# Performance work log

Hardware: AMD Instinct MI355X
Metric: run time of the kernel (lower is better)

## Reference

```python
import jax, jax.numpy as jnp
import numpy as np
from jax import lax

DIM = 128
HEADS = 8
HEAD_DIM = DIM // HEADS
SR = 2
B, H, W = 2, 80, 80
SCALE = HEAD_DIM ** (-0.5)
BN_EPS = 1e-5


def _conv1x1(x, w, b):
    # x: (B,C,H,W), w: (O,C), b: (O,)
    return jnp.einsum('bchw,oc->bohw', x, w) + b[None, :, None, None]


def setup_inputs() -> dict:
    key = jax.random.key(0)
    ks = jax.random.split(key, 12)
    s = DIM ** -0.5
    x = jax.random.normal(ks[0], (B, DIM, H, W), dtype=jnp.float32)
    q_w = jax.random.normal(ks[1], (DIM, DIM), dtype=jnp.float32) * s
    q_b = jnp.zeros((DIM,), jnp.float32)
    k_w = jax.random.normal(ks[2], (DIM, DIM), dtype=jnp.float32) * s
    k_b = jnp.zeros((DIM,), jnp.float32)
    v_w = jax.random.normal(ks[3], (DIM, DIM), dtype=jnp.float32) * s
    v_b = jnp.zeros((DIM,), jnp.float32)
    sr_w = jax.random.normal(ks[4], (DIM, DIM, SR, SR), dtype=jnp.float32) * (s / SR)
    sr_b = jnp.zeros((DIM,), jnp.float32)
    bn_gamma = jnp.ones((DIM,), jnp.float32)
    bn_beta = jnp.zeros((DIM,), jnp.float32)
    bn_mean = jnp.zeros((DIM,), jnp.float32)
    bn_var = jnp.ones((DIM,), jnp.float32)
    proj_w = jax.random.normal(ks[5], (DIM, DIM), dtype=jnp.float32) * s
    proj_b = jnp.zeros((DIM,), jnp.float32)
    return dict(x=x, q_w=q_w, q_b=q_b, k_w=k_w, k_b=k_b, v_w=v_w, v_b=v_b,
                sr_w=sr_w, sr_b=sr_b, bn_gamma=bn_gamma, bn_beta=bn_beta,
                bn_mean=bn_mean, bn_var=bn_var, proj_w=proj_w, proj_b=proj_b)


def reference(x, q_w, q_b, k_w, k_b, v_w, v_b, sr_w, sr_b,
              bn_gamma, bn_beta, bn_mean, bn_var, proj_w, proj_b):
    b, c, h, w = x.shape
    n = h * w
    # q: (B,h,N,d)
    q = _conv1x1(x, q_w, q_b).reshape(b, HEADS, HEAD_DIM, n).transpose(0, 1, 3, 2)
    # spatial reduction: Conv2d(k=SR, s=SR) + BN(eval) + ReLU
    x_kv = lax.conv_general_dilated(x, sr_w, window_strides=(SR, SR),
                                    padding='VALID',
                                    dimension_numbers=('NCHW', 'OIHW', 'NCHW'))
    x_kv = x_kv + sr_b[None, :, None, None]
    inv = bn_gamma / jnp.sqrt(bn_var + BN_EPS)
    x_kv = x_kv * inv[None, :, None, None] + (bn_beta - bn_mean * inv)[None, :, None, None]
    x_kv = jax.nn.relu(x_kv)
    n_kv = x_kv.shape[2] * x_kv.shape[3]
    k = _conv1x1(x_kv, k_w, k_b).reshape(b, HEADS, HEAD_DIM, n_kv).transpose(0, 1, 3, 2)
    v = _conv1x1(x_kv, v_w, v_b).reshape(b, HEADS, HEAD_DIM, n_kv).transpose(0, 1, 3, 2)
    # explicit attention: (B,h,N,N_kv)
    attn = jnp.einsum('bhnd,bhmd->bhnm', q, k) * SCALE
    attn = jax.nn.softmax(attn, axis=-1)
    out = jnp.einsum('bhnm,bhmd->bhnd', attn, v)  # (B,h,N,d)
    # faithful to source layout: transpose(1,2) then reshape to (B,C,H,W)
    out = out.transpose(0, 2, 1, 3).reshape(b, c, h, w)
    out = _conv1x1(out, proj_w, proj_b)
    return out
```

## Files before the change

### kernel.cpp

```cpp
#include <hip/hip_runtime.h>
#include <hip/hip_bf16.h>
#include <cmath>

#define DIM 128
#define HEADS 8
#define NBATCH 2
#define NQ 6400
#define NKV 1600
#define NC 50
#define BN_EPS 1e-5f
#define LOG2E 1.4426950408889634f

typedef __bf16 bf16_t;
typedef __attribute__((ext_vector_type(8))) __bf16 bf16x8;
typedef __attribute__((ext_vector_type(16))) float f32x16;

union BF8U { bf16x8 v; unsigned u[4]; };

__device__ inline unsigned packbf2(float a, float b) {
  union { __hip_bfloat162 v; unsigned u; } r;
  r.v = __float22bfloat162_rn(make_float2(a, b));
  return r.u;
}

__device__ inline unsigned short f2bf(float v) {
  unsigned u = __float_as_uint(v);
  return (unsigned short)((u + 0x7FFFu + ((u >> 16) & 1u)) >> 16);
}

__global__ __launch_bounds__(256) void mgemm_qsrkv(
    const float* __restrict__ x,
    const float* __restrict__ qw, const float* __restrict__ kw,
    const float* __restrict__ vw, const float* __restrict__ srw,
    const float* __restrict__ q_b, const float* __restrict__ sr_b,
    const float* __restrict__ k_b, const float* __restrict__ v_b,
    const float* __restrict__ bng, const float* __restrict__ bnb,
    const float* __restrict__ bnm, const float* __restrict__ bnv,
    unsigned short* __restrict__ Qb,
    unsigned short* __restrict__ Kp, unsigned short* __restrict__ Vp,
    float sl)
{
  __shared__ __align__(16) unsigned short xs4[32][520];
  __shared__ __align__(16) unsigned short xs[32][136];
  int t = threadIdx.x;
  int ln = t & 31, hf = (t >> 5) & 1, wid = t >> 6;
  int b = blockIdx.y;
  int o = wid * 32 + ln;

  if (blockIdx.x < 50) {
    int cid = blockIdx.x;
    int s0 = cid * 32;

    {
      int tx = t & 31, g = t >> 5;
      int s = s0 + tx;
      int i = s / 40, j = s % 40;
      const float* xb = x + (size_t)b * DIM * NQ;
#pragma unroll
      for (int u = 0; u < 32; ++u) {
        int idx2 = g * 32 + u;
        int c = idx2 >> 1, ky = idx2 & 1;
        const float* src = xb + (size_t)c * NQ + (2 * i + ky) * 80 + 2 * j;
        float2 vv = *(const float2*)src;
        *(unsigned*)&xs4[tx][c * 4 + ky * 2] = packbf2(vv.x, vv.y);
      }
    }
    __syncthreads();

    const unsigned short* arow = &xs4[ln][hf * 8];
    const float* wrow = srw + (size_t)o * 512;
    f32x16 acc = {};
#pragma unroll 8
    for (int c0 = 0; c0 < 512; c0 += 16) {
      int cb = c0 + hf * 8;
      bf16x8 af = *(const bf16x8*)&arow[c0];
      BF8U bf;
      float4 w0 = *(const float4*)(wrow + cb);
      float4 w1 = *(const float4*)(wrow + cb + 4);
      bf.u[0] = packbf2(w0.x, w0.y); bf.u[1] = packbf2(w0.z, w0.w);
      bf.u[2] = packbf2(w1.x, w1.y); bf.u[3] = packbf2(w1.z, w1.w);
      acc = __builtin_amdgcn_mfma_f32_32x32x16_bf16(af, bf.v, acc, 0, 0, 0);
    }
    float bv = sr_b[o];
    float inv = bng[o] / sqrtf(bnv[o] + BN_EPS);
    float b2 = bnb[o] - bnm[o] * inv;
#pragma unroll
    for (int g = 0; g < 4; ++g)
#pragma unroll
      for (int jj = 0; jj < 4; ++jj) {
        int sr = 8 * g + 4 * hf + jj;
        xs[sr][o] = f2bf(fmaxf((acc[4 * g + jj] + bv) * inv + b2, 0.f));
      }
    __syncthreads();

    const unsigned short* ar2 = &xs[ln][hf * 8];
    const float* kwrow = kw + (size_t)o * DIM;
    const float* vwrow = vw + (size_t)o * DIM;
    f32x16 ka = {}, va = {};
#pragma unroll
    for (int c0 = 0; c0 < 128; c0 += 16) {
      int cb = c0 + hf * 8;
      bf16x8 af = *(const bf16x8*)&ar2[c0];
      BF8U kb, vb;
      float4 k0 = *(const float4*)(kwrow + cb);
      float4 k1 = *(const float4*)(kwrow + cb + 4);
      float4 v0 = *(const float4*)(vwrow + cb);
      float4 v1 = *(const float4*)(vwrow + cb + 4);
      kb.u[0] = packbf2(k0.x, k0.y); kb.u[1] = packbf2(k0.z, k0.w);
      kb.u[2] = packbf2(k1.x, k1.y); kb.u[3] = packbf2(k1.z, k1.w);
      vb.u[0] = packbf2(v0.x, v0.y); vb.u[1] = packbf2(v0.z, v0.w);
      vb.u[2] = packbf2(v1.x, v1.y); vb.u[3] = packbf2(v1.z, v1.w);
      ka = __builtin_amdgcn_mfma_f32_32x32x16_bf16(af, kb.v, ka, 0, 0, 0);
      va = __builtin_amdgcn_mfma_f32_32x32x16_bf16(af, vb.v, va, 0, 0, 0);
    }
    int hloc = o >> 4, d = o & 15;
    {
      float kb2 = k_b[o];
      size_t CB = (((size_t)b * HEADS + hloc) * NC + cid) * 512;
#pragma unroll
      for (int g = 0; g < 4; ++g)
#pragma unroll
        for (int jj = 0; jj < 4; ++jj) {
          int sl2 = 8 * g + 4 * hf + jj;
          Kp[CB + sl2 * 16 + d] = f2bf(ka[4 * g + jj] + kb2);
        }
    }
    {
      float vb2 = v_b[o];
      size_t CB = (((size_t)b * HEADS + hloc) * NC + cid) * 1024;
      uint4 w0, w1;
      w0.x = packbf2(va[0] + vb2, va[1] + vb2);
      w0.y = packbf2(va[2] + vb2, va[3] + vb2);
      w0.z = packbf2(va[4] + vb2, va[5] + vb2);
      w0.w = packbf2(va[6] + vb2, va[7] + vb2);
      w1.x = packbf2(va[8] + vb2, va[9] + vb2);
      w1.y = packbf2(va[10] + vb2, va[11] + vb2);
      w1.z = packbf2(va[12] + vb2, va[13] + vb2);
      w1.w = packbf2(va[14] + vb2, va[15] + vb2);
      *(uint4*)&Vp[CB + d * 16 + hf * 8] = w0;
      *(uint4*)&Vp[CB + 512 + d * 16 + hf * 8] = w1;
    }
    {
      int hh = t >> 5, pos = t & 31;
      size_t addr = (((size_t)b * HEADS + hh) * NC + cid) * 1024 + 256 +
                    ((pos & 16) ? 512 : 0) + (pos & 15);
      Vp[addr] = 0x3F80;
    }
  } else {
    int s0 = (blockIdx.x - 50) * 32;

    {
      int tx = t & 31, cg = t >> 5;
      const float* xb = x + (size_t)b * DIM * NQ + s0 + tx;
#pragma unroll
      for (int it = 0; it < 8; ++it) {
        int c = 2 * cg + 16 * it;
        float a0 = xb[(size_t)c * NQ];
        float a1 = xb[(size_t)(c + 1) * NQ];
        *(unsigned*)&xs[tx][c] = packbf2(a0, a1);
      }
    }
    __syncthreads();

    const unsigned short* arow = &xs[ln][hf * 8];
    const float* qwrow = qw + (size_t)o * DIM;
    f32x16 acc = {};
#pragma unroll
    for (int c0 = 0; c0 < 128; c0 += 16) {
      int cb = c0 + hf * 8;
      bf16x8 af = *(const bf16x8*)&arow[c0];
      BF8U bf;
      float4 b0 = *(const float4*)(qwrow + cb);
      float4 b1 = *(const float4*)(qwrow + cb + 4);
      bf.u[0] = packbf2(b0.x, b0.y); bf.u[1] = packbf2(b0.z, b0.w);
      bf.u[2] = packbf2(b1.x, b1.y); bf.u[3] = packbf2(b1.z, b1.w);
      acc = __builtin_amdgcn_mfma_f32_32x32x16_bf16(af, bf.v, acc, 0, 0, 0);
    }
    float bv = q_b[o];
#pragma unroll
    for (int g = 0; g < 4; ++g)
#pragma unroll
      for (int jj = 0; jj < 4; ++jj) {
        int sq = s0 + 8 * g + 4 * hf + jj;
        Qb[((size_t)b * NQ + sq) * DIM + o] = f2bf((acc[4 * g + jj] + bv) * sl);
      }
  }
}

__global__ __launch_bounds__(256) void attn_split(
    const bf16_t* __restrict__ Qb, const bf16_t* __restrict__ Kp,
    const bf16_t* __restrict__ Vp, unsigned short* __restrict__ Pb,
    float* __restrict__ Lsum)
{
  const int t = threadIdx.x;
  const int ln = t & 31, hf = (t >> 5) & 1, wid = t >> 6;
  const int h = blockIdx.y;
  const int b = blockIdx.z & 1, half = blockIdx.z >> 1;
  const int q0 = blockIdx.x * 128 + wid * 32;

  bf16x8 qf = *(const bf16x8*)&Qb[((size_t)b * NQ + q0 + ln) * DIM + h * 16 + hf * 8];
  const int bh = b * HEADS + h;
  const bf16_t* kc = &Kp[((size_t)bh * NC + half * 25) * 512 + ln * 16 + hf * 8];
  const bf16_t* vc = &Vp[((size_t)bh * NC + half * 25) * 1024 + ln * 16 + hf * 8];

  f32x16 acc0 = {}, acc1 = {};
  const f32x16 zero = {};

  bf16x8 kf0 = *(const bf16x8*)kc;
  bf16x8 va0 = *(const bf16x8*)vc;
  bf16x8 vb0 = *(const bf16x8*)(vc + 512);
  bf16x8 kf1 = *(const bf16x8*)(kc + 512);
  bf16x8 va1 = *(const bf16x8*)(vc + 1024);
  bf16x8 vb1 = *(const bf16x8*)(vc + 1536);

  f32x16 S0 = __builtin_amdgcn_mfma_f32_32x32x16_bf16(kf0, qf, zero, 0, 0, 0);

  for (int c = 0; c < 25; ++c) {
    int cn = (c + 2 < 25) ? c + 2 : 24;
    bf16x8 kf2 = *(const bf16x8*)(kc + (size_t)cn * 512);
    bf16x8 va2 = *(const bf16x8*)(vc + (size_t)cn * 1024);
    bf16x8 vb2 = *(const bf16x8*)(vc + (size_t)cn * 1024 + 512);

    f32x16 S1 = __builtin_amdgcn_mfma_f32_32x32x16_bf16(kf1, qf, zero, 0, 0, 0);

    BF8U f0, f1;
#pragma unroll
    for (int i = 0; i < 4; ++i) {
      f0.u[i] = packbf2(__builtin_amdgcn_exp2f(S0[2 * i]),
                        __builtin_amdgcn_exp2f(S0[2 * i + 1]));
      f1.u[i] = packbf2(__builtin_amdgcn_exp2f(S0[8 + 2 * i]),
                        __builtin_amdgcn_exp2f(S0[9 + 2 * i]));
    }

    acc0 = __builtin_amdgcn_mfma_f32_32x32x16_bf16(va0, f0.v, acc0, 0, 0, 0);
    acc1 = __builtin_amdgcn_mfma_f32_32x32x16_bf16(vb0, f1.v, acc1, 0, 0, 0);

    S0 = S1;
    kf0 = kf1; va0 = va1; vb0 = vb1;
    kf1 = kf2; va1 = va2; vb1 = vb2;
  }

  f32x16 acc;
#pragma unroll
  for (int i = 0; i < 16; ++i) acc[i] = acc0[i] + acc1[i];

  unsigned short* prow =
      &Pb[(size_t)(half * 2 + b) * (NQ * DIM) + (size_t)(q0 + ln) * DIM + h * 16 + 4 * hf];
  uint2 w0, w1;
  w0.x = packbf2(acc[0], acc[1]); w0.y = packbf2(acc[2], acc[3]);
  w1.x = packbf2(acc[4], acc[5]); w1.y = packbf2(acc[6], acc[7]);
  *(uint2*)&prow[0] = w0;
  *(uint2*)&prow[8] = w1;
  if (!hf)
    Lsum[(size_t)(half * 2 + b) * (HEADS * NQ) + (size_t)h * NQ + q0 + ln] = acc[8];
}

__global__ __launch_bounds__(256) void proj_comb(
    const unsigned short* __restrict__ Pb, const float* __restrict__ Lsum,
    const float* __restrict__ pw, const float* __restrict__ p_b,
    float* __restrict__ Out)
{
  __shared__ __align__(16) unsigned short As[32][136];
  int t = threadIdx.x;
  int b = blockIdx.y;
  int s0 = blockIdx.x * 32;

  {
    int tx = t & 31, cg = t >> 5;
#pragma unroll
    for (int it = 0; it < 16; ++it) {
      int c = cg * 16 + it;
      int f = c * NQ + s0 + tx;
      int n = f >> 7, hh = (f >> 4) & 7;
      float p0 = __uint_as_float((unsigned)Pb[(size_t)b * (NQ * DIM) + f] << 16);
      float p1 = __uint_as_float((unsigned)Pb[(size_t)(2 + b) * (NQ * DIM) + f] << 16);
      float L = Lsum[(size_t)b * (HEADS * NQ) + (size_t)hh * NQ + n] +
                Lsum[(size_t)(2 + b) * (HEADS * NQ) + (size_t)hh * NQ + n];
      As[tx][c] = f2bf((p0 + p1) / L);
    }
  }
  __syncthreads();

  int ln = t & 31, hf = (t >> 5) & 1, wid = t >> 6;
  int o = wid * 32 + ln;
  const float* brow = pw + (size_t)o * DIM;
  const unsigned short* arow = &As[ln][hf * 8];
  f32x16 acc = {};
#pragma unroll
  for (int c0 = 0; c0 < 128; c0 += 16) {
    int cb = c0 + hf * 8;
    bf16x8 af = *(const bf16x8*)&arow[c0];
    BF8U bf;
    float4 b0 = *(const float4*)(brow + cb);
    float4 b1 = *(const float4*)(brow + cb + 4);
    bf.u[0] = packbf2(b0.x, b0.y); bf.u[1] = packbf2(b0.z, b0.w);
    bf.u[2] = packbf2(b1.x, b1.y); bf.u[3] = packbf2(b1.z, b1.w);
    acc = __builtin_amdgcn_mfma_f32_32x32x16_bf16(af, bf.v, acc, 0, 0, 0);
  }
  float bv = p_b[o];
  float* obase = &Out[((size_t)b * DIM + o) * NQ + s0 + 4 * hf];
#pragma unroll
  for (int g = 0; g < 4; ++g) {
    float4 r;
    r.x = acc[4 * g + 0] + bv; r.y = acc[4 * g + 1] + bv;
    r.z = acc[4 * g + 2] + bv; r.w = acc[4 * g + 3] + bv;
    *(float4*)&obase[8 * g] = r;
  }
}

extern "C" void kernel_launch(void* const* d_in, const int* in_sizes, int n_in,
                              void* d_out, int out_size, void* d_ws, size_t ws_size,
                              hipStream_t stream)
{
  const float* x    = (const float*)d_in[0];
  const float* q_w  = (const float*)d_in[1];
  const float* q_b  = (const float*)d_in[2];
  const float* k_w  = (const float*)d_in[3];
  const float* k_b  = (const float*)d_in[4];
  const float* v_w  = (const float*)d_in[5];
  const float* v_b  = (const float*)d_in[6];
  const float* sr_w = (const float*)d_in[7];
  const float* sr_b = (const float*)d_in[8];
  const float* bng  = (const float*)d_in[9];
  const float* bnb  = (const float*)d_in[10];
  const float* bnm  = (const float*)d_in[11];
  const float* bnv  = (const float*)d_in[12];
  const float* p_w  = (const float*)d_in[13];
  const float* p_b  = (const float*)d_in[14];
  float* out = (float*)d_out;

  float* ws = (float*)d_ws;
  bf16_t* Qb   = (bf16_t*)(ws);
  bf16_t* Kp   = (bf16_t*)(ws + 819200);
  bf16_t* Vp   = (bf16_t*)(ws + 1024000);
  float*  Lsum = ws + 1433600;
  bf16_t* Pb   = (bf16_t*)(ws + 1638400);

  const float sl = 0.25f * LOG2E;

  mgemm_qsrkv<<<dim3(250, NBATCH), dim3(256), 0, stream>>>(
      x, q_w, k_w, v_w, sr_w, q_b, sr_b, k_b, v_b, bng, bnb, bnm, bnv,
      (unsigned short*)Qb, (unsigned short*)Kp, (unsigned short*)Vp, sl);

  attn_split<<<dim3(NQ / 128, HEADS, 4), dim3(256), 0, stream>>>(
      Qb, Kp, Vp, (unsigned short*)Pb, Lsum);

  proj_comb<<<dim3(200, NBATCH), dim3(256), 0, stream>>>(
      (const unsigned short*)Pb, Lsum, p_w, p_b, out);
}
```

Before: 155.2 us.

## Precast weights to bf16, process two query tiles per attention block, pair Pb loads

Adds a kernel that converts all weight matrices to bf16 once per call, so the GEMM kernels load ready bf16 fragments instead of converting fp32 inside their inner loops. The attention kernel now computes two 128-query tiles per block, reusing each loaded K/V chunk twice and halving the grid. The projection kernel reads Pb two elements at a time. The change adds one kernel launch, raises register pressure in attention and reduces the number of attention blocks.

Result: faster. 145.1 us (-6.5%).

```diff
diff --git a/kernel.cpp b/kernel.cpp
--- a/kernel.cpp
+++ b/kernel.cpp
@@ -28,10 +28,27 @@
   return (unsigned short)((u + 0x7FFFu + ((u >> 16) & 1u)) >> 16);
 }
 
+__global__ __launch_bounds__(256) void wcast(
+    const float* __restrict__ qw, const float* __restrict__ kw,
+    const float* __restrict__ vw, const float* __restrict__ pw,
+    const float* __restrict__ srw, unsigned short* __restrict__ Wb)
+{
+  int e4 = (blockIdx.x * 256 + threadIdx.x) * 4;
+  const float* src; int idx;
+  if (e4 < 16384)      { src = qw;  idx = e4; }
+  else if (e4 < 32768) { src = kw;  idx = e4 - 16384; }
+  else if (e4 < 49152) { src = vw;  idx = e4 - 32768; }
+  else if (e4 < 65536) { src = pw;  idx = e4 - 49152; }
+  else                 { src = srw; idx = e4 - 65536; }
+  float4 v = *(const float4*)(src + idx);
+  uint2 wv;
+  wv.x = packbf2(v.x, v.y);
+  wv.y = packbf2(v.z, v.w);
+  *(uint2*)&Wb[e4] = wv;
+}
+
 __global__ __launch_bounds__(256) void mgemm_qsrkv(
-    const float* __restrict__ x,
-    const float* __restrict__ qw, const float* __restrict__ kw,
-    const float* __restrict__ vw, const float* __restrict__ srw,
+    const float* __restrict__ x, const bf16_t* __restrict__ Wb,
     const float* __restrict__ q_b, const float* __restrict__ sr_b,
     const float* __restrict__ k_b, const float* __restrict__ v_b,
     const float* __restrict__ bng, const float* __restrict__ bnb,
@@ -68,18 +85,13 @@
     __syncthreads();
 
     const unsigned short* arow = &xs4[ln][hf * 8];
-    const float* wrow = srw + (size_t)o * 512;
+    const bf16_t* brow = &Wb[65536 + (size_t)o * 512 + hf * 8];
     f32x16 acc = {};
 #pragma unroll 8
     for (int c0 = 0; c0 < 512; c0 += 16) {
-      int cb = c0 + hf * 8;
       bf16x8 af = *(const bf16x8*)&arow[c0];
-      BF8U bf;
-      float4 w0 = *(const float4*)(wrow + cb);
-      float4 w1 = *(const float4*)(wrow + cb + 4);
-      bf.u[0] = packbf2(w0.x, w0.y); bf.u[1] = packbf2(w0.z, w0.w);
-      bf.u[2] = packbf2(w1.x, w1.y); bf.u[3] = packbf2(w1.z, w1.w);
-      acc = __builtin_amdgcn_mfma_f32_32x32x16_bf16(af, bf.v, acc, 0, 0, 0);
+      bf16x8 bf = *(const bf16x8*)&brow[c0];
+      acc = __builtin_amdgcn_mfma_f32_32x32x16_bf16(af, bf, acc, 0, 0, 0);
     }
     float bv = sr_b[o];
     float inv = bng[o] / sqrtf(bnv[o] + BN_EPS);
@@ -94,24 +106,16 @@
     __syncthreads();
 
     const unsigned short* ar2 = &xs[ln][hf * 8];
-    const float* kwrow = kw + (size_t)o * DIM;
-    const float* vwrow = vw + (size_t)o * DIM;
+    const bf16_t* kbrow = &Wb[16384 + (size_t)o * DIM + hf * 8];
+    const bf16_t* vbrow = &Wb[32768 + (size_t)o * DIM + hf * 8];
     f32x16 ka = {}, va = {};
 #pragma unroll
     for (int c0 = 0; c0 < 128; c0 += 16) {
-      int cb = c0 + hf * 8;
       bf16x8 af = *(const bf16x8*)&ar2[c0];
-      BF8U kb, vb;
-      float4 k0 = *(const float4*)(kwrow + cb);
-      float4 k1 = *(const float4*)(kwrow + cb + 4);
-      float4 v0 = *(const float4*)(vwrow + cb);
-      float4 v1 = *(const float4*)(vwrow + cb + 4);
-      kb.u[0] = packbf2(k0.x, k0.y); kb.u[1] = packbf2(k0.z, k0.w);
-      kb.u[2] = packbf2(k1.x, k1.y); kb.u[3] = packbf2(k1.z, k1.w);
-      vb.u[0] = packbf2(v0.x, v0.y); vb.u[1] = packbf2(v0.z, v0.w);
-      vb.u[2] = packbf2(v1.x, v1.y); vb.u[3] = packbf2(v1.z, v1.w);
-      ka = __builtin_amdgcn_mfma_f32_32x32x16_bf16(af, kb.v, ka, 0, 0, 0);
-      va = __builtin_amdgcn_mfma_f32_32x32x16_bf16(af, vb.v, va, 0, 0, 0);
+      bf16x8 kb = *(const bf16x8*)&kbrow[c0];
+      bf16x8 vb = *(const bf16x8*)&vbrow[c0];
+      ka = __builtin_amdgcn_mfma_f32_32x32x16_bf16(af, kb, ka, 0, 0, 0);
+      va = __builtin_amdgcn_mfma_f32_32x32x16_bf16(af, vb, va, 0, 0, 0);
     }
     int hloc = o >> 4, d = o & 15;
     {
@@ -163,18 +167,13 @@
     __syncthreads();
 
     const unsigned short* arow = &xs[ln][hf * 8];
-    const float* qwrow = qw + (size_t)o * DIM;
+    const bf16_t* brow = &Wb[(size_t)o * DIM + hf * 8];
     f32x16 acc = {};
 #pragma unroll
     for (int c0 = 0; c0 < 128; c0 += 16) {
-      int cb = c0 + hf * 8;
       bf16x8 af = *(const bf16x8*)&arow[c0];
-      BF8U bf;
-      float4 b0 = *(const float4*)(qwrow + cb);
-      float4 b1 = *(const float4*)(qwrow + cb + 4);
-      bf.u[0] = packbf2(b0.x, b0.y); bf.u[1] = packbf2(b0.z, b0.w);
-      bf.u[2] = packbf2(b1.x, b1.y); bf.u[3] = packbf2(b1.z, b1.w);
-      acc = __builtin_amdgcn_mfma_f32_32x32x16_bf16(af, bf.v, acc, 0, 0, 0);
+      bf16x8 bf = *(const bf16x8*)&brow[c0];
+      acc = __builtin_amdgcn_mfma_f32_32x32x16_bf16(af, bf, acc, 0, 0, 0);
     }
     float bv = q_b[o];
 #pragma unroll
@@ -196,14 +195,16 @@
   const int ln = t & 31, hf = (t >> 5) & 1, wid = t >> 6;
   const int h = blockIdx.y;
   const int b = blockIdx.z & 1, half = blockIdx.z >> 1;
-  const int q0 = blockIdx.x * 128 + wid * 32;
-
-  bf16x8 qf = *(const bf16x8*)&Qb[((size_t)b * NQ + q0 + ln) * DIM + h * 16 + hf * 8];
+  const int q0 = blockIdx.x * 256 + wid * 32;
+  const int q1 = q0 + 128;
+
+  bf16x8 qfA = *(const bf16x8*)&Qb[((size_t)b * NQ + q0 + ln) * DIM + h * 16 + hf * 8];
+  bf16x8 qfB = *(const bf16x8*)&Qb[((size_t)b * NQ + q1 + ln) * DIM + h * 16 + hf * 8];
   const int bh = b * HEADS + h;
   const bf16_t* kc = &Kp[((size_t)bh * NC + half * 25) * 512 + ln * 16 + hf * 8];
   const bf16_t* vc = &Vp[((size_t)bh * NC + half * 25) * 1024 + ln * 16 + hf * 8];
 
-  f32x16 acc0 = {}, acc1 = {};
+  f32x16 aA0 = {}, aA1 = {}, aB0 = {}, aB1 = {};
   const f32x16 zero = {};
 
   bf16x8 kf0 = *(const bf16x8*)kc;
@@ -213,7 +214,8 @@
   bf16x8 va1 = *(const bf16x8*)(vc + 1024);
   bf16x8 vb1 = *(const bf16x8*)(vc + 1536);
 
-  f32x16 S0 = __builtin_amdgcn_mfma_f32_32x32x16_bf16(kf0, qf, zero, 0, 0, 0);
+  f32x16 S0a = __builtin_amdgcn_mfma_f32_32x32x16_bf16(kf0, qfA, zero, 0, 0, 0);
+  f32x16 S0b = __builtin_amdgcn_mfma_f32_32x32x16_bf16(kf0, qfB, zero, 0, 0, 0);
 
   for (int c = 0; c < 25; ++c) {
     int cn = (c + 2 < 25) ? c + 2 : 24;
@@ -221,43 +223,70 @@
     bf16x8 va2 = *(const bf16x8*)(vc + (size_t)cn * 1024);
     bf16x8 vb2 = *(const bf16x8*)(vc + (size_t)cn * 1024 + 512);
 
-    f32x16 S1 = __builtin_amdgcn_mfma_f32_32x32x16_bf16(kf1, qf, zero, 0, 0, 0);
-
-    BF8U f0, f1;
-#pragma unroll
-    for (int i = 0; i < 4; ++i) {
-      f0.u[i] = packbf2(__builtin_amdgcn_exp2f(S0[2 * i]),
-                        __builtin_amdgcn_exp2f(S0[2 * i + 1]));
-      f1.u[i] = packbf2(__builtin_amdgcn_exp2f(S0[8 + 2 * i]),
-                        __builtin_amdgcn_exp2f(S0[9 + 2 * i]));
-    }
-
-    acc0 = __builtin_amdgcn_mfma_f32_32x32x16_bf16(va0, f0.v, acc0, 0, 0, 0);
-    acc1 = __builtin_amdgcn_mfma_f32_32x32x16_bf16(vb0, f1.v, acc1, 0, 0, 0);
-
-    S0 = S1;
+    f32x16 S1a = __builtin_amdgcn_mfma_f32_32x32x16_bf16(kf1, qfA, zero, 0, 0, 0);
+    f32x16 S1b = __builtin_amdgcn_mfma_f32_32x32x16_bf16(kf1, qfB, zero, 0, 0, 0);
+
+    {
+      BF8U f0, f1;
+#pragma unroll
+      for (int i = 0; i < 4; ++i) {
+        f0.u[i] = packbf2(__builtin_amdgcn_exp2f(S0a[2 * i]),
+                          __builtin_amdgcn_exp2f(S0a[2 * i + 1]));
+        f1.u[i] = packbf2(__builtin_amdgcn_exp2f(S0a[8 + 2 * i]),
+                          __builtin_amdgcn_exp2f(S0a[9 + 2 * i]));
+      }
+      aA0 = __builtin_amdgcn_mfma_f32_32x32x16_bf16(va0, f0.v, aA0, 0, 0, 0);
+      aA1 = __builtin_amdgcn_mfma_f32_32x32x16_bf16(vb0, f1.v, aA1, 0, 0, 0);
+    }
+    {
+      BF8U f0, f1;
+#pragma unroll
+      for (int i = 0; i < 4; ++i) {
+        f0.u[i] = packbf2(__builtin_amdgcn_exp2f(S0b[2 * i]),
+                          __builtin_amdgcn_exp2f(S0b[2 * i + 1]));
+        f1.u[i] = packbf2(__builtin_amdgcn_exp2f(S0b[8 + 2 * i]),
+                          __builtin_amdgcn_exp2f(S0b[9 + 2 * i]));
+      }
+      aB0 = __builtin_amdgcn_mfma_f32_32x32x16_bf16(va0, f0.v, aB0, 0, 0, 0);
+      aB1 = __builtin_amdgcn_mfma_f32_32x32x16_bf16(vb0, f1.v, aB1, 0, 0, 0);
+    }
+
+    S0a = S1a; S0b = S1b;
     kf0 = kf1; va0 = va1; vb0 = vb1;
     kf1 = kf2; va1 = va2; vb1 = vb2;
   }
 
-  f32x16 acc;
-#pragma unroll
-  for (int i = 0; i < 16; ++i) acc[i] = acc0[i] + acc1[i];
-
-  unsigned short* prow =
-      &Pb[(size_t)(half * 2 + b) * (NQ * DIM) + (size_t)(q0 + ln) * DIM + h * 16 + 4 * hf];
-  uint2 w0, w1;
-  w0.x = packbf2(acc[0], acc[1]); w0.y = packbf2(acc[2], acc[3]);
-  w1.x = packbf2(acc[4], acc[5]); w1.y = packbf2(acc[6], acc[7]);
-  *(uint2*)&prow[0] = w0;
-  *(uint2*)&prow[8] = w1;
-  if (!hf)
-    Lsum[(size_t)(half * 2 + b) * (HEADS * NQ) + (size_t)h * NQ + q0 + ln] = acc[8];
+  f32x16 accA, accB;
+#pragma unroll
+  for (int i = 0; i < 16; ++i) { accA[i] = aA0[i] + aA1[i]; accB[i] = aB0[i] + aB1[i]; }
+
+  size_t sbase = (size_t)(half * 2 + b) * (NQ * DIM);
+  {
+    unsigned short* prow = &Pb[sbase + (size_t)(q0 + ln) * DIM + h * 16 + 4 * hf];
+    uint2 w0, w1;
+    w0.x = packbf2(accA[0], accA[1]); w0.y = packbf2(accA[2], accA[3]);
+    w1.x = packbf2(accA[4], accA[5]); w1.y = packbf2(accA[6], accA[7]);
+    *(uint2*)&prow[0] = w0;
+    *(uint2*)&prow[8] = w1;
+  }
+  {
+    unsigned short* prow = &Pb[sbase + (size_t)(q1 + ln) * DIM + h * 16 + 4 * hf];
+    uint2 w0, w1;
+    w0.x = packbf2(accB[0], accB[1]); w0.y = packbf2(accB[2], accB[3]);
+    w1.x = packbf2(accB[4], accB[5]); w1.y = packbf2(accB[6], accB[7]);
+    *(uint2*)&prow[0] = w0;
+    *(uint2*)&prow[8] = w1;
+  }
+  if (!hf) {
+    size_t lbase = (size_t)(half * 2 + b) * (HEADS * NQ) + (size_t)h * NQ;
+    Lsum[lbase + q0 + ln] = accA[8];
+    Lsum[lbase + q1 + ln] = accB[8];
+  }
 }
 
 __global__ __launch_bounds__(256) void proj_comb(
     const unsigned short* __restrict__ Pb, const float* __restrict__ Lsum,
-    const float* __restrict__ pw, const float* __restrict__ p_b,
+    const bf16_t* __restrict__ Wb, const float* __restrict__ p_b,
     float* __restrict__ Out)
 {
   __shared__ __align__(16) unsigned short As[32][136];
@@ -266,36 +295,36 @@
   int s0 = blockIdx.x * 32;
 
   {
-    int tx = t & 31, cg = t >> 5;
-#pragma unroll
-    for (int it = 0; it < 16; ++it) {
-      int c = cg * 16 + it;
-      int f = c * NQ + s0 + tx;
+    int tp = t & 15, cg = t >> 4;
+    const unsigned short* p0base = Pb + (size_t)b * (NQ * DIM);
+    const unsigned short* p1base = Pb + (size_t)(2 + b) * (NQ * DIM);
+#pragma unroll
+    for (int it = 0; it < 8; ++it) {
+      int c = cg * 8 + it;
+      int f = c * NQ + s0 + 2 * tp;
       int n = f >> 7, hh = (f >> 4) & 7;
-      float p0 = __uint_as_float((unsigned)Pb[(size_t)b * (NQ * DIM) + f] << 16);
-      float p1 = __uint_as_float((unsigned)Pb[(size_t)(2 + b) * (NQ * DIM) + f] << 16);
+      unsigned u0 = *(const unsigned*)&p0base[f];
+      unsigned u1 = *(const unsigned*)&p1base[f];
       float L = Lsum[(size_t)b * (HEADS * NQ) + (size_t)hh * NQ + n] +
                 Lsum[(size_t)(2 + b) * (HEADS * NQ) + (size_t)hh * NQ + n];
-      As[tx][c] = f2bf((p0 + p1) / L);
+      float plo = __uint_as_float(u0 << 16) + __uint_as_float(u1 << 16);
+      float phi = __uint_as_float(u0 & 0xFFFF0000u) + __uint_as_float(u1 & 0xFFFF0000u);
+      As[2 * tp][c]     = f2bf(plo / L);
+      As[2 * tp + 1][c] = f2bf(phi / L);
     }
   }
   __syncthreads();
 
   int ln = t & 31, hf = (t >> 5) & 1, wid = t >> 6;
   int o = wid * 32 + ln;
-  const float* brow = pw + (size_t)o * DIM;
+  const bf16_t* brow = &Wb[49152 + (size_t)o * DIM + hf * 8];
   const unsigned short* arow = &As[ln][hf * 8];
   f32x16 acc = {};
 #pragma unroll
   for (int c0 = 0; c0 < 128; c0 += 16) {
-    int cb = c0 + hf * 8;
     bf16x8 af = *(const bf16x8*)&arow[c0];
-    BF8U bf;
-    float4 b0 = *(const float4*)(brow + cb);
-    float4 b1 = *(const float4*)(brow + cb + 4);
-    bf.u[0] = packbf2(b0.x, b0.y); bf.u[1] = packbf2(b0.z, b0.w);
-    bf.u[2] = packbf2(b1.x, b1.y); bf.u[3] = packbf2(b1.z, b1.w);
-    acc = __builtin_amdgcn_mfma_f32_32x32x16_bf16(af, bf.v, acc, 0, 0, 0);
+    bf16x8 bf = *(const bf16x8*)&brow[c0];
+    acc = __builtin_amdgcn_mfma_f32_32x32x16_bf16(af, bf, acc, 0, 0, 0);
   }
   float bv = p_b[o];
   float* obase = &Out[((size_t)b * DIM + o) * NQ + s0 + 4 * hf];
@@ -335,16 +364,20 @@
   bf16_t* Vp   = (bf16_t*)(ws + 1024000);
   float*  Lsum = ws + 1433600;
   bf16_t* Pb   = (bf16_t*)(ws + 1638400);
+  bf16_t* Wb   = (bf16_t*)(ws + 3276800);
 
   const float sl = 0.25f * LOG2E;
 
+  wcast<<<dim3(128), dim3(256), 0, stream>>>(
+      q_w, k_w, v_w, p_w, sr_w, (unsigned short*)Wb);
+
   mgemm_qsrkv<<<dim3(250, NBATCH), dim3(256), 0, stream>>>(
-      x, q_w, k_w, v_w, sr_w, q_b, sr_b, k_b, v_b, bng, bnb, bnm, bnv,
+      x, Wb, q_b, sr_b, k_b, v_b, bng, bnb, bnm, bnv,
       (unsigned short*)Qb, (unsigned short*)Kp, (unsigned short*)Vp, sl);
 
-  attn_split<<<dim3(NQ / 128, HEADS, 4), dim3(256), 0, stream>>>(
+  attn_split<<<dim3(NQ / 256, HEADS, 4), dim3(256), 0, stream>>>(
       Qb, Kp, Vp, (unsigned short*)Pb, Lsum);
 
   proj_comb<<<dim3(200, NBATCH), dim3(256), 0, stream>>>(
-      (const unsigned short*)Pb, Lsum, p_w, p_b, out);
-}
+      (const unsigned short*)Pb, Lsum, Wb, p_b, out);
+}
```
